# Kernel optimization log

Measured on AMD Instinct MI355X. Metric: run time of the kernel, lower is better.

Reference implementation:

```python
import jax, jax.numpy as jnp
import numpy as np

B, L, D = 2, 4096, 1024
H, DK, DV = 4, 256, 256
CONV_K = 4
FIR_KS = (1, 3, 7, 15)
GQP = 128
NS = len(FIR_KS) + 2  # fir scales + delta path + direct value path
GIN = GQP + NS
GH = max(8, GIN)
CHUNK = 32
FLOOR = 0.02  # step 0 -> floor_start


def l2norm(x):
    return x * jax.lax.rsqrt(jnp.sum(x * x, -1, keepdims=True) + 1e-6)


def dw_causal_conv(x, w):
    # x: (B, L, C), w: (C, K) depthwise causal conv (ShortConvolution / FIR)
    K = w.shape[1]
    y = jax.lax.conv_general_dilated(
        jnp.moveaxis(x, 1, 2), w[:, None, :], (1,), [(K - 1, 0)],
        feature_group_count=w.shape[0],
        dimension_numbers=("NCH", "OIH", "NCH"))
    return jnp.moveaxis(y, 1, 2)


def delta_rule_chunkwise(q, k, v, beta):
    # q,k: (b,h,L,dk)  v: (b,h,L,dv)  beta: (b,h,L);  L % CHUNK == 0
    b, h, Lp, dk = q.shape
    dv = v.shape[-1]
    n = Lp // CHUNK
    q = l2norm(q)
    k = l2norm(k)
    v = v * beta[..., None]
    kb = k * beta[..., None]
    rs = lambda t: t.reshape(b, h, n, CHUNK, -1)
    q, k, v, kb = rs(q), rs(k), rs(v), rs(kb)
    tri = jnp.triu(jnp.ones((CHUNK, CHUNK), bool), 0)       # incl diag
    tri_s = jnp.triu(jnp.ones((CHUNK, CHUNK), bool), 1)     # strict upper
    # inv = -(k_beta k^T) masked to strictly-lower
    inv = -jnp.where(tri, 0.0, jnp.einsum('bhncd,bhned->bhnce', kb, k))
    # forward substitution: (I - A)^{-1} - I for strictly lower A
    for i in range(1, CHUNK):
        row = inv[:, :, :, i, :]                              # (b,h,n,C)
        upd = jnp.einsum('bhnk,bhnkj->bhnj', row, inv)        # zero for j>=i
        inv = inv.at[:, :, :, i, :].add(upd)
    inv = inv + jnp.eye(CHUNK, dtype=inv.dtype)
    inv = inv.astype(jnp.bfloat16).astype(q.dtype)
    u = inv @ v                                               # (b,h,n,C,dv)
    w = inv @ kb                                              # (b,h,n,C,dk)
    mv = lambda t: jnp.moveaxis(t, 2, 0)                      # -> (n,b,h,C,d)
    S0 = jnp.zeros((b, h, dk, dv), q.dtype)

    def step(S, xs):
        q_i, k_i, u_i, w_i = xs
        attn = jnp.where(tri_s, 0.0, q_i @ jnp.swapaxes(k_i, -1, -2))
        u_t = u_i - w_i @ S
        o = q_i @ S + attn @ u_t
        S = S + jnp.swapaxes(k_i, -1, -2) @ u_t
        return S, o

    _, out = jax.lax.scan(step, S0, (mv(q), mv(k), mv(u), mv(w)))
    return jnp.moveaxis(out, 0, 2).reshape(b, h, Lp, dv)


def rmsnorm(x, w, eps=1e-5):
    return x * jax.lax.rsqrt(jnp.mean(x * x, -1, keepdims=True) + eps) * w


def _dirac_fir(key, channels, k):
    w = jnp.zeros((channels, k), jnp.float32).at[:, -1].set(1.0)
    return w + 0.01 * jax.random.normal(key, (channels, k), jnp.float32)


def setup_inputs():
    key = jax.random.key(0)
    ks = jax.random.split(key, 24)
    sc = 0.02
    C = H * DV
    b2 = jnp.zeros((NS,), jnp.float32).at[-1].set(1.0)  # identity-path bias
    return {
        "hidden_states": jax.random.normal(ks[0], (B, L, D), jnp.float32),
        "Wq": jax.random.normal(ks[1], (D, H * DK), jnp.float32) * sc,
        "Wk": jax.random.normal(ks[2], (D, H * DK), jnp.float32) * sc,
        "Wv": jax.random.normal(ks[3], (D, H * DV), jnp.float32) * sc,
        "Wb": jax.random.normal(ks[4], (D, H), jnp.float32) * sc,
        "conv_q_w": jax.random.normal(ks[5], (H * DK, CONV_K), jnp.float32) * 0.1,
        "conv_k_w": jax.random.normal(ks[6], (H * DK, CONV_K), jnp.float32) * 0.1,
        "conv_v_w": jax.random.normal(ks[7], (H * DV, CONV_K), jnp.float32) * 0.1,
        "fir_w0": _dirac_fir(ks[8], C, FIR_KS[0]),
        "fir_w1": _dirac_fir(ks[9], C, FIR_KS[1]),
        "fir_w2": _dirac_fir(ks[10], C, FIR_KS[2]),
        "fir_w3": _dirac_fir(ks[11], C, FIR_KS[3]),
        "Wqg": jax.random.normal(ks[12], (D, GQP), jnp.float32) * sc,
        "bqg": jnp.zeros((GQP,), jnp.float32),
        "Wf1": jax.random.normal(ks[13], (GIN, GH), jnp.float32) * sc,
        "bf1": jnp.zeros((GH,), jnp.float32),
        "Wf2": jax.random.normal(ks[14], (GH, NS), jnp.float32) * sc,
        "bf2": b2,
        "log_temp": jnp.zeros((H,), jnp.float32),
        "o_norm_w": jnp.ones((DV,), jnp.float32),
        "Wo": jax.random.normal(ks[15], (H * DV, D), jnp.float32) * sc,
    }


def reference(hidden_states, Wq, Wk, Wv, Wb, conv_q_w, conv_k_w, conv_v_w,
              fir_w0, fir_w1, fir_w2, fir_w3, Wqg, bqg, Wf1, bf1, Wf2, bf2,
              log_temp, o_norm_w, Wo):
    x = hidden_states
    # projections + causal ShortConvolution with SiLU (qk_activation='silu')
    q = jax.nn.silu(dw_causal_conv(x @ Wq, conv_q_w))
    k = jax.nn.silu(dw_causal_conv(x @ Wk, conv_k_w))
    v = jax.nn.silu(dw_causal_conv(x @ Wv, conv_v_w))
    q = q.reshape(B, L, H, DK)
    k = k.reshape(B, L, H, DK)
    v_direct = v.reshape(B, L, H, DV)
    beta = jax.nn.sigmoid(x @ Wb)  # (B,L,H)
    bh = lambda t: jnp.swapaxes(t, 1, 2)  # (B,L,H,d) -> (B,H,L,d)
    delta_bh = delta_rule_chunkwise(bh(q), bh(k), bh(v_direct), jnp.swapaxes(beta, 1, 2))
    delta_out = jnp.swapaxes(delta_bh, 1, 2)  # (B,L,H,DV)
    # multi-scale depthwise causal FIR branches on the value stream
    v_flat = v_direct.reshape(B, L, H * DV)
    firs = [dw_causal_conv(v_flat, w).reshape(B, L, H, DV)
            for w in (fir_w0, fir_w1, fir_w2, fir_w3)]
    streams = jnp.stack(firs + [delta_out, v_direct], axis=3)  # (B,L,H,NS,DV)
    # query-conditioned summary router
    summaries = jnp.mean(streams, axis=-1)                     # (B,L,H,NS)
    qg = x @ Wqg + bqg                                         # (B,L,GQP)
    qg = jnp.broadcast_to(qg[:, :, None, :], (B, L, H, GQP))
    gate_in = jnp.concatenate([qg, summaries], axis=-1)        # (B,L,H,GIN)
    hmid = jax.nn.gelu(gate_in @ Wf1 + bf1, approximate=False)
    logits = (hmid @ Wf2 + bf2) / jnp.exp(log_temp)[None, None, :, None]
    p = jax.nn.softmax(logits, axis=-1)
    p = p * (1.0 - NS * FLOOR) + FLOOR                          # prob floor
    fused = jnp.einsum('blhs,blhsd->blhd', p, streams)
    o = rmsnorm(fused, o_norm_w)
    return o.reshape(B, L, H * DV) @ Wo
```

## Files before the change

kernel.cpp:

```cpp
#include <hip/hip_runtime.h>
#include <hip/hip_bf16.h>
#include <math.h>

#define B_ 2
#define L_ 4096
#define D_ 1024
#define H_ 4
#define DK_ 256
#define BL_ 8192
#define C_ 1024
#define NCH_ 128
#define GQP_c 128
#define NS_c 6
#define GIN_c 134
#define GH_c 134

typedef __attribute__((ext_vector_type(8))) short short8;
typedef __attribute__((ext_vector_type(4))) float f32x4;

__device__ __forceinline__ float block_sum256(float v, float* red) {
  int t = threadIdx.x;
  #pragma unroll
  for (int o = 32; o > 0; o >>= 1) v += __shfl_down(v, o, 64);
  __syncthreads();
// ... 142 lines not shown
  const float* xr = x + (size_t)row * D_;
  float acc = 0.f;
  for (int k = lane; k < D_; k += 64) acc += xr[k] * Wb[(k << 2) + h];
  #pragma unroll
  for (int o = 32; o > 0; o >>= 1) acc += __shfl_down(acc, o, 64);
  if (lane == 0) beta[(row << 2) + h] = 1.f / (1.f + expf(-acc));
}

__global__ __launch_bounds__(256) void precompute(const float* __restrict__ q,
    const float* __restrict__ k, const float* __restrict__ v,
    const float* __restrict__ beta,
    float* __restrict__ qn, float* __restrict__ kn,
    float* __restrict__ vb, float* __restrict__ kb) {
  __shared__ float red[4];
  int bid = blockIdx.x;
  int t = threadIdx.x;
  int b = bid >> 14;
  int h = (bid >> 12) & 3;
  int l = bid & (L_ - 1);
  size_t in_off = (((size_t)(b * L_ + l)) << 10) + (h << 8) + t;
  float qv = q[in_off], kv = k[in_off], vv = v[in_off];
  float sq = block_sum256(qv * qv, red);
  float sk = block_sum256(kv * kv, red);
  float rq = rsqrtf(sq + 1e-6f);
  float rk = rsqrtf(sk + 1e-6f);
  float bt = beta[((b * L_ + l) << 2) + h];
  size_t oo = ((size_t)bid << 8) + t;
  float knv = kv * rk;
  qn[oo] = qv * rq;
  kn[oo] = knv;
  vb[oo] = vv * bt;
  kb[oo] = knv * bt;
}

__global__ __launch_bounds__(256) void inv_attn(const float* __restrict__ qn,
    const float* kn, const float* __restrict__ kb,
    float* __restrict__ invb, __hip_bfloat16* __restrict__ att_bf,
    __hip_bfloat16* knT_bf) {
  __shared__ float kn_s[32][257];
  __shared__ float inv_s[32][33];
  int ci = blockIdx.x;
  int t = threadIdx.x;
  size_t base = ((size_t)ci) << 13;
  for (int e = t; e < 8192; e += 256) kn_s[e >> 8][e & 255] = kn[base + e];
  __syncthreads();
  {
    unsigned short tmp[32];
    #pragma unroll
    for (int j = 0; j < 32; ++j) tmp[j] = bf16bits(kn_s[j][t]);
    unsigned short* kd = (unsigned short*)knT_bf + (((size_t)ci) << 14) +
                         (size_t)(t >> 4) * 512 + (size_t)(t & 15) * 8;
    #pragma unroll
    for (int g = 0; g < 4; ++g) *(uint4*)(kd + g * 128) = ((const uint4*)tmp)[g];
  }
  {
    int r = t >> 3, kt = t & 7;
    const float4* qrow = (const float4*)(qn + base + (size_t)r * 256 + (kt << 5));
    unsigned short tmp[32];
    #pragma unroll
    for (int i = 0; i < 8; ++i) {
      float4 f = qrow[i];
      tmp[i * 4 + 0] = bf16bits(f.x); tmp[i * 4 + 1] = bf16bits(f.y);
      tmp[i * 4 + 2] = bf16bits(f.z); tmp[i * 4 + 3] = bf16bits(f.w);
    }
    unsigned short* qd = (unsigned short*)knT_bf + (((size_t)ci) << 14) + 8192 +
                         (size_t)(((r >> 4) << 3) + kt) * 512 + (size_t)(r & 15) * 8;
    #pragma unroll
    for (int g = 0; g < 4; ++g) *(uint4*)(qd + g * 128) = ((const uint4*)tmp)[g];
  }
  #pragma unroll
  for (int p = 0; p < 4; ++p) {
    int e = t + (p << 8);
    int i = e >> 5, j = e & 31;
    const float* kbi = kb + base + (i << 8);
    const float* qni = qn + base + (i << 8);
    float am = 0.f, aa = 0.f;
    for (int kk = 0; kk < 256; ++kk) {
      float knv = kn_s[j][kk];
      am += kbi[kk] * knv;
      aa += qni[kk] * knv;
    }
    inv_s[i][j] = (j < i) ? -am : 0.f;
    ((unsigned short*)att_bf)[((size_t)ci << 10) + (size_t)(i >> 4) * 512 +
        (size_t)((i & 15) + ((j >> 3) << 4)) * 8 + (j & 7)] =
        bf16bits((j <= i) ? aa : 0.f);
  }
  __syncthreads();
  for (int i = 1; i < 32; ++i) {
    float upd = 0.f;
    if (t < i) {
      for (int kk = t + 1; kk < i; ++kk) upd += inv_s[i][kk] * inv_s[kk][t];
    }
    __syncthreads();
    if (t < i) inv_s[i][t] += upd;
    __syncthreads();
  }
  #pragma unroll
  for (int p = 0; p < 4; ++p) {
    int e = t + (p << 8);
    int i = e >> 5, j = e & 31;
    float val = inv_s[i][j] + (i == j ? 1.f : 0.f);
    val = __bfloat162float(__float2bfloat16(val));
    invb[((size_t)ci << 10) + e] = val;
  }
}

__global__ __launch_bounds__(256) void uw_kernel(const float* __restrict__ invb,
    float* __restrict__ vb_u, float* kb_w, __hip_bfloat16* w_bf) {
  __shared__ float inv_s[32][33];
  __shared__ float tile[32][260];
  int ci = blockIdx.x, t = threadIdx.x;
  size_t base = ((size_t)ci) << 13;
  for (int e = t; e < 1024; e += 256) inv_s[e >> 5][e & 31] = invb[((size_t)ci << 10) + e];
  for (int ph = 0; ph < 2; ++ph) {
    const float* src = (ph == 0) ? vb_u : kb_w;
    __syncthreads();
    for (int f = t; f < 2048; f += 256) {
      int e = f << 2;
      *(float4*)&tile[e >> 8][e & 255] = *(const float4*)(src + base + e);
    }
    __syncthreads();
    int c4 = (t & 63) << 2;
    int ig = t >> 6;
    float4 acc[8];
    #pragma unroll
    for (int ii = 0; ii < 8; ++ii) acc[ii] = make_float4(0.f, 0.f, 0.f, 0.f);
    for (int j = 0; j < 32; ++j) {
      float4 v4 = *(const float4*)&tile[j][c4];
      #pragma unroll
      for (int ii = 0; ii < 8; ++ii) {
        float iv = inv_s[(ig << 3) + ii][j];
        acc[ii].x += iv * v4.x; acc[ii].y += iv * v4.y;
        acc[ii].z += iv * v4.z; acc[ii].w += iv * v4.w;
      }
    }
    #pragma unroll
    for (int ii = 0; ii < 8; ++ii) {
      int i = (ig << 3) + ii;
      if (ph == 0) {
        *(float4*)(vb_u + base + (i << 8) + c4) = acc[ii];
      } else {
        ushort4 o;
        o.x = bf16bits(-acc[ii].x); o.y = bf16bits(-acc[ii].y);
        o.z = bf16bits(-acc[ii].z); o.w = bf16bits(-acc[ii].w);
        unsigned short* wd = (unsigned short*)w_bf + (((size_t)ci) << 14) +
            (size_t)(((i >> 4) << 3) + (c4 >> 5)) * 512 +
            (size_t)((i & 15) + (((c4 >> 3) & 3) << 4)) * 8 + (c4 & 7);
        *(ushort4*)wd = o;
      }
    }
  }
}

__global__ __launch_bounds__(64, 1) void scan_kernel(
    const __hip_bfloat16* __restrict__ w_bf,
    const __hip_bfloat16* __restrict__ kq_bf,
    const __hip_bfloat16* __restrict__ att_bf,
    const float* __restrict__ u, float* __restrict__ dout) {
  __shared__ __align__(16) unsigned short Sim[2][2][16 * 264];
  __shared__ __align__(16) float UtT[16 * 36];
  int lane = threadIdx.x;
  int mlane = lane & 15, quad = lane >> 4;
  int bh = blockIdx.x & 7;
  int cb = blockIdx.x >> 3;
  int cbase = cb << 4;

  const unsigned short* wbase = (const unsigned short*)w_bf;
  const unsigned short* kqbase = (const unsigned short*)kq_bf;
  const unsigned short* abase = (const unsigned short*)att_bf;

  short8 Wr[16], Qr[16], Kr[16], Ar[2];
  float ur[8], urn[8];

  auto load_WQ = [&](int nc) {
    size_t cb14 = ((size_t)(bh * NCH_ + nc)) << 14;
    const short8* wg = (const short8*)(wbase + cb14 + (size_t)lane * 8);
    const short8* qg = (const short8*)(kqbase + cb14 + 8192 + (size_t)lane * 8);
    #pragma unroll
    for (int s = 0; s < 16; ++s) { Wr[s] = wg[s * 64]; Qr[s] = qg[s * 64]; }
  };
  auto load_K = [&](int nc) {
    size_t cb14 = ((size_t)(bh * NCH_ + nc)) << 14;
    const short8* kg = (const short8*)(kqbase + cb14 + (size_t)lane * 8);
    #pragma unroll
    for (int s = 0; s < 16; ++s) Kr[s] = kg[s * 64];
  };
  auto load_A = [&](int nc) {
    const short8* ag = (const short8*)(abase + (((size_t)(bh * NCH_ + nc)) << 10) +
                                       (size_t)lane * 8);
    Ar[0] = ag[0]; Ar[1] = ag[64];
  };
  auto load_u8 = [&](int nc, float* dst) {
    size_t cbf = ((size_t)(bh * NCH_ + nc)) << 13;
    const float* up = u + cbf + (size_t)(quad * 4) * 256 + cbase + mlane;
    #pragma unroll
    for (int tt = 0; tt < 2; ++tt)
      #pragma unroll
      for (int r = 0; r < 4; ++r) dst[tt * 4 + r] = up[(tt * 16 + r) * 256];
  };

  for (int e = lane; e < 16 * 264; e += 64) { Sim[0][0][e] = 0; Sim[0][1][e] = 0; }
  f32x4 accS[16];
  #pragma unroll
  for (int i = 0; i < 16; ++i) accS[i] = (f32x4){0.f, 0.f, 0.f, 0.f};

  load_WQ(0);
  load_K(0);
  load_A(0);
  load_u8(0, ur);

  for (int nc = 0; nc < NCH_; ++nc) {
    int cur = nc & 1, alt = cur ^ 1;
    int nn = nc + 1 < NCH_ ? nc + 1 : NCH_ - 1;

    f32x4 uh0 = (f32x4){ur[0], ur[1], ur[2], ur[3]};
    f32x4 uh1 = (f32x4){ur[4], ur[5], ur[6], ur[7]};
    f32x4 ul0 = (f32x4){0.f, 0.f, 0.f, 0.f}, ul1 = (f32x4){0.f, 0.f, 0.f, 0.f};
    f32x4 oh0 = (f32x4){0.f, 0.f, 0.f, 0.f}, oh1 = (f32x4){0.f, 0.f, 0.f, 0.f};
    f32x4 ol0 = (f32x4){0.f, 0.f, 0.f, 0.f}, ol1 = (f32x4){0.f, 0.f, 0.f, 0.f};
    #pragma unroll
    for (int kt = 0; kt < 8; ++kt) {
      short8 bhi = *(const short8*)&Sim[cur][0][mlane * 264 + kt * 32 + quad * 8];
      short8 blo = *(const short8*)&Sim[cur][1][mlane * 264 + kt * 32 + quad * 8];
      uh0 = __builtin_amdgcn_mfma_f32_16x16x32_bf16(Wr[kt], bhi, uh0, 0, 0, 0);
      ul0 = __builtin_amdgcn_mfma_f32_16x16x32_bf16(Wr[kt], blo, ul0, 0, 0, 0);
      uh1 = __builtin_amdgcn_mfma_f32_16x16x32_bf16(Wr[8 + kt], bhi, uh1, 0, 0, 0);
      ul1 = __builtin_amdgcn_mfma_f32_16x16x32_bf16(Wr[8 + kt], blo, ul1, 0, 0, 0);
      oh0 = __builtin_amdgcn_mfma_f32_16x16x32_bf16(Qr[kt], bhi, oh0, 0, 0, 0);
      ol0 = __builtin_amdgcn_mfma_f32_16x16x32_bf16(Qr[kt], blo, ol0, 0, 0, 0);
      oh1 = __builtin_amdgcn_mfma_f32_16x16x32_bf16(Qr[8 + kt], bhi, oh1, 0, 0, 0);
      ol1 = __builtin_amdgcn_mfma_f32_16x16x32_bf16(Qr[8 + kt], blo, ol1, 0, 0, 0);
    }
    f32x4 ut0 = uh0 + ul0, ut1 = uh1 + ul1;
    *(f32x4*)&UtT[mlane * 36 + quad * 4] = ut0;
    *(f32x4*)&UtT[mlane * 36 + 16 + quad * 4] = ut1;
    load_WQ(nn);
    load_u8(nn, urn);
    short8 but;
    {
      const float* up = &UtT[mlane * 36 + quad * 8];
      #pragma unroll
      for (int j = 0; j < 8; ++j) but[j] = (short)bf16bits(up[j]);
    }
    f32x4 o0 = oh0 + ol0, o1 = oh1 + ol1;
    o0 = __builtin_amdgcn_mfma_f32_16x16x32_bf16(Ar[0], but, o0, 0, 0, 0);
    o1 = __builtin_amdgcn_mfma_f32_16x16x32_bf16(Ar[1], but, o1, 0, 0, 0);
    load_A(nn);
    size_t cbf = ((size_t)(bh * NCH_ + nc)) << 13;
    float* op = dout + cbf + (size_t)(quad * 4) * 256 + cbase + mlane;
    #pragma unroll
    for (int r = 0; r < 4; ++r) { op[r * 256] = o0[r]; op[(16 + r) * 256] = o1[r]; }
    #pragma unroll
    for (int t2 = 0; t2 < 16; ++t2) {
      accS[t2] = __builtin_amdgcn_mfma_f32_16x16x32_bf16(Kr[t2], but, accS[t2], 0, 0, 0);
      unsigned short nh[4], nl[4];
      #pragma unroll
      for (int r = 0; r < 4; ++r) {
        float sv = accS[t2][r];
        unsigned short hb = bf16bits(sv);
        nh[r] = hb;
        nl[r] = bf16bits(sv - bits2f(hb));
      }
      *(uint2*)&Sim[alt][0][mlane * 264 + t2 * 16 + quad * 4] = *(const uint2*)nh;
      *(uint2*)&Sim[alt][1][mlane * 264 + t2 * 16 + quad * 4] = *(const uint2*)nl;
    }
    load_K(nn);
    #pragma unroll
    for (int r = 0; r < 8; ++r) ur[r] = urn[r];
  }
}

__global__ __launch_bounds__(256, 1) void gate_kernel(
    const float* __restrict__ v, const float* __restrict__ delta,
    const float* __restrict__ qgH,
    const float* __restrict__ fw0, const float* __restrict__ fw1T,
    const float* __restrict__ fw2T, const float* __restrict__ fw3T,
    const float* __restrict__ Wf1, const float* __restrict__ Wf2,
    const float* __restrict__ bf1, const float* __restrict__ bf2,
    const float* __restrict__ ltm, const float* __restrict__ onw,
    __hip_bfloat16* __restrict__ obf) {
  __shared__ float W1t[6][136];
  __shared__ float W2f[804];
  __shared__ float bf1s[136];
  int t = threadIdx.x;
  int wave = t >> 6, lane = t & 63;
  for (int e = t; e < 804; e += 256) {
    int s = e / 134, u = e - s * 134;
    W1t[s][u] = Wf1[(128 + s) * GH_c + u];
    W2f[e] = Wf2[e];
  }
  if (t < GH_c) bf1s[t] = bf1[t];
  __syncthreads();

  int bid = blockIdx.x;
  int bl0 = (((bid & 7) << 7) | (bid >> 3)) << 3;
  int b = bl0 >> 12;
  int h = wave;
  int c = (h << 8) + (lane << 2);

  float4 fw3r[15], fw2r[7], fw1r[3], fw0r;
  #pragma unroll
  for (int j = 0; j < 15; ++j) fw3r[j] = *(const float4*)(fw3T + (j << 10) + c);
  #pragma unroll
  for (int j = 0; j < 7; ++j) fw2r[j] = *(const float4*)(fw2T + (j << 10) + c);
  #pragma unroll
  for (int j = 0; j < 3; ++j) fw1r[j] = *(const float4*)(fw1T + (j << 10) + c);
  fw0r = *(const float4*)(fw0 + c);
  float4 ow = *(const float4*)(onw + (lane << 2));
  float itemp = expf(ltm[h]);
  float b2r[6];
  #pragma unroll
  for (int s = 0; s < 6; ++s) b2r[s] = bf2[s];
  int u3 = 128 + (lane < 6 ? lane : 0);

  auto gelu = [](float a) -> float {
    return 0.5f * a * (1.f + erff(a * 0.70710678f));
  };

  for (int tk = 0; tk < 8; ++tk) {
    int bl = bl0 + tk;
    int l = bl & (L_ - 1);
    float4 st0, st1, st2, st3, st4, st5;
    st1 = make_float4(0, 0, 0, 0);
    st2 = make_float4(0, 0, 0, 0);
    st3 = make_float4(0, 0, 0, 0);
    #pragma unroll
    for (int j = 0; j < 15; ++j) {
      int ll = l - 14 + j;
      float4 vj = make_float4(0, 0, 0, 0);
      if (ll >= 0) vj = *(const float4*)(v + ((((size_t)(b * L_ + ll)) << 10) + c));
      st3 = fma4(fw3r[j], vj, st3);
      if (j >= 8) st2 = fma4(fw2r[j - 8], vj, st2);
      if (j >= 12) st1 = fma4(fw1r[j - 12], vj, st1);
      if (j == 14) {
        st0 = make_float4(fw0r.x * vj.x, fw0r.y * vj.y, fw0r.z * vj.z, fw0r.w * vj.w);
        st5 = vj;
      }
    }
    st4 = *(const float4*)(delta + ((((size_t)((b * H_ + h) * L_ + l)) << 8) + (lane << 2)));

    float s0 = st0.x + st0.y + st0.z + st0.w;
    float s1 = st1.x + st1.y + st1.z + st1.w;
    float s2 = st2.x + st2.y + st2.z + st2.w;
    float s3 = st3.x + st3.y + st3.z + st3.w;
    float s4 = st4.x + st4.y + st4.z + st4.w;
    float s5 = st5.x + st5.y + st5.z + st5.w;
    #pragma unroll
    for (int o = 32; o > 0; o >>= 1) {
      s0 += __shfl_down(s0, o, 64); s1 += __shfl_down(s1, o, 64);
      s2 += __shfl_down(s2, o, 64); s3 += __shfl_down(s3, o, 64);
      s4 += __shfl_down(s4, o, 64); s5 += __shfl_down(s5, o, 64);
    }
    float ss_[6];
    ss_[0] = __shfl(s0, 0, 64) * (1.f / 256.f);
    ss_[1] = __shfl(s1, 0, 64) * (1.f / 256.f);
    ss_[2] = __shfl(s2, 0, 64) * (1.f / 256.f);
    ss_[3] = __shfl(s3, 0, 64) * (1.f / 256.f);
    ss_[4] = __shfl(s4, 0, 64) * (1.f / 256.f);
    ss_[5] = __shfl(s5, 0, 64) * (1.f / 256.f);

    const float* qr = qgH + ((size_t)bl << 8);
    float a0 = qr[lane] + bf1s[lane];
    float a1 = qr[64 + lane] + bf1s[64 + lane];
    float a2 = qr[u3] + bf1s[u3];
    #pragma unroll
    for (int s = 0; s < 6; ++s) {
      a0 = fmaf(W1t[s][lane], ss_[s], a0);
      a1 = fmaf(W1t[s][64 + lane], ss_[s], a1);
      a2 = fmaf(W1t[s][u3], ss_[s], a2);
    }
    float h0 = gelu(a0);
    float h1 = gelu(a1);
    float h2 = (lane < 6) ? gelu(a2) : 0.f;

    const float* w2a = W2f + lane * 6;
    const float* w2b = W2f + (64 + lane) * 6;
    const float* w2c = W2f + u3 * 6;
    float t0 = h0 * w2a[0] + h1 * w2b[0] + h2 * w2c[0];
    float t1 = h0 * w2a[1] + h1 * w2b[1] + h2 * w2c[1];
    float t2 = h0 * w2a[2] + h1 * w2b[2] + h2 * w2c[2];
    float t3 = h0 * w2a[3] + h1 * w2b[3] + h2 * w2c[3];
    float t4 = h0 * w2a[4] + h1 * w2b[4] + h2 * w2c[4];
    float t5 = h0 * w2a[5] + h1 * w2b[5] + h2 * w2c[5];
    #pragma unroll
    for (int o = 32; o > 0; o >>= 1) {
      t0 += __shfl_down(t0, o, 64); t1 += __shfl_down(t1, o, 64);
      t2 += __shfl_down(t2, o, 64); t3 += __shfl_down(t3, o, 64);
      t4 += __shfl_down(t4, o, 64); t5 += __shfl_down(t5, o, 64);
    }
    float p0, p1, p2, p3, p4, p5;
    if (lane == 0) {
      float l0v = (t0 + b2r[0]) / itemp, l1v = (t1 + b2r[1]) / itemp;
      float l2v = (t2 + b2r[2]) / itemp, l3v = (t3 + b2r[3]) / itemp;
      float l4v = (t4 + b2r[4]) / itemp, l5v = (t5 + b2r[5]) / itemp;
      float m = fmaxf(fmaxf(fmaxf(l0v, l1v), fmaxf(l2v, l3v)), fmaxf(l4v, l5v));
      float e0 = expf(l0v - m), e1 = expf(l1v - m), e2 = expf(l2v - m);
      float e3 = expf(l3v - m), e4 = expf(l4v - m), e5 = expf(l5v - m);
      float inv = 1.f / (e0 + e1 + e2 + e3 + e4 + e5);
      p0 = e0 * inv * 0.88f + 0.02f; p1 = e1 * inv * 0.88f + 0.02f;
      p2 = e2 * inv * 0.88f + 0.02f; p3 = e3 * inv * 0.88f + 0.02f;
      p4 = e4 * inv * 0.88f + 0.02f; p5 = e5 * inv * 0.88f + 0.02f;
    }
    p0 = __shfl(p0, 0, 64); p1 = __shfl(p1, 0, 64); p2 = __shfl(p2, 0, 64);
    p3 = __shfl(p3, 0, 64); p4 = __shfl(p4, 0, 64); p5 = __shfl(p5, 0, 64);

    float4 fu;
    fu.x = p0 * st0.x + p1 * st1.x + p2 * st2.x + p3 * st3.x + p4 * st4.x + p5 * st5.x;
    fu.y = p0 * st0.y + p1 * st1.y + p2 * st2.y + p3 * st3.y + p4 * st4.y + p5 * st5.y;
    fu.z = p0 * st0.z + p1 * st1.z + p2 * st2.z + p3 * st3.z + p4 * st4.z + p5 * st5.z;
    fu.w = p0 * st0.w + p1 * st1.w + p2 * st2.w + p3 * st3.w + p4 * st4.w + p5 * st5.w;
    float ssq = fu.x * fu.x + fu.y * fu.y + fu.z * fu.z + fu.w * fu.w;
    #pragma unroll
    for (int o = 32; o > 0; o >>= 1) ssq += __shfl_xor(ssq, o, 64);
    float sc = rsqrtf(ssq * (1.f / 256.f) + 1e-5f);
    ushort4 ob;
    ob.x = bf16bits(fu.x * sc * ow.x);
    ob.y = bf16bits(fu.y * sc * ow.y);
    ob.z = bf16bits(fu.z * sc * ow.z);
    ob.w = bf16bits(fu.w * sc * ow.w);
    *(ushort4*)((unsigned short*)obf + (((size_t)bl) << 10) + c) = ob;
  }
}

extern "C" void kernel_launch(void* const* d_in, const int* in_sizes, int n_in,
                              void* d_out, int out_size, void* d_ws, size_t ws_size,
                              hipStream_t stream) {
  const float* x   = (const float*)d_in[0];
  const float* Wq  = (const float*)d_in[1];
  const float* Wk  = (const float*)d_in[2];
  const float* Wv  = (const float*)d_in[3];
  const float* Wb  = (const float*)d_in[4];
  const float* cqw = (const float*)d_in[5];
  const float* ckw = (const float*)d_in[6];
  const float* cvw = (const float*)d_in[7];
  const float* fw0 = (const float*)d_in[8];
  const float* fw1 = (const float*)d_in[9];
  const float* fw2 = (const float*)d_in[10];
  const float* fw3 = (const float*)d_in[11];
  const float* Wqg = (const float*)d_in[12];
  const float* bqg = (const float*)d_in[13];
  const float* Wf1 = (const float*)d_in[14];
  const float* bf1 = (const float*)d_in[15];
  const float* Wf2 = (const float*)d_in[16];
  const float* bf2 = (const float*)d_in[17];
  const float* ltm = (const float*)d_in[18];
  const float* onw = (const float*)d_in[19];
  const float* Wo  = (const float*)d_in[20];
  float* out = (float*)d_out;
  float* ws = (float*)d_ws;

  const size_t BIG = (size_t)BL_ * C_;
  float* qpre = ws;
  float* kpre = ws + BIG;
  float* vpre = ws + 2 * BIG;
  float* qs   = ws + 3 * BIG;
  float* ks   = ws + 4 * BIG;
  float* vs   = ws + 5 * BIG;
  float* kbw  = ws + 6 * BIG;
  float* invb = ws + 7 * BIG;
  float* attb = invb + (size_t)1024 * 1024;
  float* beta = attb + (size_t)1024 * 1024;
  float* qg   = beta + (size_t)BL_ * H_;

  __hip_bfloat16* x_bf  = (__hip_bfloat16*)qs;
  __hip_bfloat16* wqT   = (__hip_bfloat16*)kbw;
  __hip_bfloat16* wkT   = wqT + (size_t)1024 * 1024;
  __hip_bfloat16* wvT   = wkT + (size_t)1024 * 1024;
  __hip_bfloat16* wqgT  = wvT + (size_t)1024 * 1024;
  __hip_bfloat16* woT   = (__hip_bfloat16*)kbw;
  __hip_bfloat16* gate_bf = (__hip_bfloat16*)qpre;
  __hip_bfloat16* knT_bf = (__hip_bfloat16*)kpre;
  __hip_bfloat16* w_bf   = (__hip_bfloat16*)kbw;
  __hip_bfloat16* att_bf = (__hip_bfloat16*)attb;
  float* scr   = attb + (size_t)600000;
  float* fw1T  = scr;
  float* fw2T  = scr + 3072;
  float* fw3T  = scr + 10240;

  float* qgH = ks;
  __hip_bfloat16* qg_bf  = (__hip_bfloat16*)(ks + (size_t)3 * 1024 * 1024);
  __hip_bfloat16* wf1qT  = (__hip_bfloat16*)(ks + (size_t)4 * 1024 * 1024);

  dim3 blk(256);
  f32_to_bf16_k<<<dim3(BL_ * D_ / 1024), blk, 0, stream>>>(x, x_bf);
  transpose_bf16<<<dim3(32, 32), blk, 0, stream>>>(Wq, wqT, D_, C_);
  transpose_bf16<<<dim3(32, 32), blk, 0, stream>>>(Wk, wkT, D_, C_);
  transpose_bf16<<<dim3(32, 32), blk, 0, stream>>>(Wv, wvT, D_, C_);
  transpose_bf16<<<dim3(4, 32), blk, 0, stream>>>(Wqg, wqgT, D_, GQP_c);
  small_transpose<<<dim3(16), blk, 0, stream>>>(fw1, fw1T, 1024, 3, 1024);
  small_transpose<<<dim3(32), blk, 0, stream>>>(fw2, fw2T, 1024, 7, 1024);
  small_transpose<<<dim3(64), blk, 0, stream>>>(fw3, fw3T, 1024, 15, 1024);
  gemm_bf16<<<dim3(8, 64), blk, 0, stream>>>(x_bf, wqT, nullptr, qpre, BL_, C_, D_);
  gemm_bf16<<<dim3(8, 64), blk, 0, stream>>>(x_bf, wkT, nullptr, kpre, BL_, C_, D_);
  gemm_bf16<<<dim3(8, 64), blk, 0, stream>>>(x_bf, wvT, nullptr, vpre, BL_, C_, D_);
  gemm_bf16<<<dim3(1, 64), blk, 0, stream>>>(x_bf, wqgT, bqg, qg, BL_, GQP_c, D_);
  beta_kernel<<<dim3(BL_), blk, 0, stream>>>(x, Wb, beta);
  conv_silu<<<dim3(BL_ * C_ / 256), blk, 0, stream>>>(qpre, cqw, qs);
  conv_silu<<<dim3(BL_ * C_ / 256), blk, 0, stream>>>(kpre, ckw, ks);
  conv_silu<<<dim3(BL_ * C_ / 256), blk, 0, stream>>>(vpre, cvw, vs);
  precompute<<<dim3(B_ * H_ * L_), blk, 0, stream>>>(qs, ks, vs, beta, qpre, kpre,
                                                     vpre, kbw);
  f32_to_bf16_k<<<dim3(BL_ * GQP_c / 1024), blk, 0, stream>>>(qg, qg_bf);
  wf1q_prep<<<dim3(128), blk, 0, stream>>>(Wf1, wf1qT);
  gemm_bf16<<<dim3(2, 64), blk, 0, stream>>>(qg_bf, wf1qT, nullptr, qgH, BL_, 256, 128);
  inv_attn<<<dim3(1024), blk, 0, stream>>>(qpre, kpre, kbw, invb, att_bf, knT_bf);
  uw_kernel<<<dim3(1024), blk, 0, stream>>>(invb, vpre, kbw, w_bf);
  scan_kernel<<<dim3(128), dim3(64), 0, stream>>>(w_bf, knT_bf, att_bf, vpre, qs);
  transpose_bf16<<<dim3(32, 32), blk, 0, stream>>>(Wo, woT, C_, D_);
  gate_kernel<<<dim3(1024), blk, 0, stream>>>(vs, qs, qgH, fw0, fw1T, fw2T, fw3T,
                                              Wf1, Wf2, bf1, bf2, ltm, onw, gate_bf);
  gemm_bf16<<<dim3(8, 64), blk, 0, stream>>>(gate_bf, woT, nullptr, out, BL_, D_, C_);
}
```

Measured before the change: 976.5 us.

## Process chunk pairs in scan using precomputed cross-chunk correction matrices

```diff
diff --git a/kernel.cpp b/kernel.cpp
--- a/kernel.cpp
+++ b/kernel.cpp
@@ -318,12 +318,53 @@
   }
 }
 
+__global__ __launch_bounds__(256) void mn_prep(
+    const __hip_bfloat16* __restrict__ w_bf, const __hip_bfloat16* __restrict__ kq_bf,
+    unsigned short* __restrict__ mn) {
+  __shared__ float wb_[32][260];
+  __shared__ float qb_[32][260];
+  __shared__ float ka_[256][33];
+  int p = blockIdx.x;
+  int bh = p >> 6, i = p & 63;
+  int ca = bh * NCH_ + 2 * i, cbk = ca + 1;
+  int t = threadIdx.x;
+  const unsigned short* wsrc = (const unsigned short*)w_bf + ((size_t)cbk << 14);
+  const unsigned short* qsrc = (const unsigned short*)kq_bf + ((size_t)cbk << 14) + 8192;
+  const unsigned short* ksrc = (const unsigned short*)kq_bf + ((size_t)ca << 14);
+  for (int e = t; e < 8192; e += 256) {
+    int s = e >> 9, ln = (e >> 3) & 63, j = e & 7;
+    int row = ((s >> 3) << 4) | (ln & 15);
+    int col = ((s & 7) << 5) | (((ln >> 4) & 3) << 3) | j;
+    wb_[row][col] = bits2f(wsrc[e]);
+    qb_[row][col] = bits2f(qsrc[e]);
+    int krow = (s << 4) | (ln & 15);
+    int kcol = (((ln >> 4) & 3) << 3) | j;
+    ka_[krow][kcol] = bits2f(ksrc[e]);
+  }
+  __syncthreads();
+  unsigned short* dst = mn + ((size_t)p << 11);
+  #pragma unroll
+  for (int g = 0; g < 8; ++g) {
+    int idx = g * 256 + t;
+    int which = idx >> 10;
+    int rc = idx & 1023;
+    int r = rc >> 5, ccol = rc & 31;
+    const float* src = which ? &qb_[r][0] : &wb_[r][0];
+    float acc = 0.f;
+    for (int d = 0; d < 256; ++d) acc = fmaf(src[d], ka_[d][ccol], acc);
+    int addr = ((r >> 4) << 9) + (((r & 15) | (((ccol >> 3) & 3) << 4)) << 3) + (ccol & 7);
+    dst[(which << 10) + addr] = bf16bits(acc);
+  }
+}
+
 __global__ __launch_bounds__(64, 1) void scan_kernel(
     const __hip_bfloat16* __restrict__ w_bf,
     const __hip_bfloat16* __restrict__ kq_bf,
     const __hip_bfloat16* __restrict__ att_bf,
+    const unsigned short* __restrict__ mn,
     const float* __restrict__ u, float* __restrict__ dout) {
-  __shared__ __align__(16) unsigned short Sim[2][2][16 * 264];
+  __shared__ __align__(16) unsigned short Shi[16 * 264];
+  __shared__ __align__(16) unsigned short Slo[16 * 264];
   __shared__ __align__(16) float UtT[16 * 36];
   int lane = threadIdx.x;
   int mlane = lane & 15, quad = lane >> 4;
@@ -335,59 +376,79 @@
   const unsigned short* kqbase = (const unsigned short*)kq_bf;
   const unsigned short* abase = (const unsigned short*)att_bf;
 
-  short8 Wr[16], Qr[16], Kr[16], Ar[2];
-  float ur[8], urn[8];
-
-  auto load_WQ = [&](int nc) {
-    size_t cb14 = ((size_t)(bh * NCH_ + nc)) << 14;
-    const short8* wg = (const short8*)(wbase + cb14 + (size_t)lane * 8);
-    const short8* qg = (const short8*)(kqbase + cb14 + 8192 + (size_t)lane * 8);
-    #pragma unroll
-    for (int s = 0; s < 16; ++s) { Wr[s] = wg[s * 64]; Qr[s] = qg[s * 64]; }
+  short8 Wr[16], Qr[16], Wb2[16], Qb2[16], Ka[16], Kb[16];
+  short8 Mr[2], Nr[2], Aa[2], Ab[2];
+  float ua[8], ub[8];
+
+  auto load_WQ = [&](int ci, short8* W, short8* Q) {
+    size_t c14 = ((size_t)ci) << 14;
+    const short8* wg = (const short8*)(wbase + c14 + (size_t)lane * 8);
+    const short8* qg = (const short8*)(kqbase + c14 + 8192 + (size_t)lane * 8);
+    #pragma unroll
+    for (int s = 0; s < 16; ++s) { W[s] = wg[s * 64]; Q[s] = qg[s * 64]; }
   };
-  auto load_K = [&](int nc) {
-    size_t cb14 = ((size_t)(bh * NCH_ + nc)) << 14;
-    const short8* kg = (const short8*)(kqbase + cb14 + (size_t)lane * 8);
-    #pragma unroll
-    for (int s = 0; s < 16; ++s) Kr[s] = kg[s * 64];
+  auto load_K = [&](int ci, short8* K) {
+    const short8* kg = (const short8*)(kqbase + (((size_t)ci) << 14) + (size_t)lane * 8);
+    #pragma unroll
+    for (int s = 0; s < 16; ++s) K[s] = kg[s * 64];
   };
-  auto load_A = [&](int nc) {
-    const short8* ag = (const short8*)(abase + (((size_t)(bh * NCH_ + nc)) << 10) +
+  auto load_MNA = [&](int pi) {
+    int ca = bh * NCH_ + 2 * pi, cbk = ca + 1;
+    const short8* mg = (const short8*)(mn + (((size_t)(bh * 64 + pi)) << 11) +
                                        (size_t)lane * 8);
-    Ar[0] = ag[0]; Ar[1] = ag[64];
+    Mr[0] = mg[0]; Mr[1] = mg[64];
+    Nr[0] = mg[128]; Nr[1] = mg[192];
+    const short8* aga = (const short8*)(abase + (((size_t)ca) << 10) + (size_t)lane * 8);
+    const short8* agb = (const short8*)(abase + (((size_t)cbk) << 10) + (size_t)lane * 8);
+    Aa[0] = aga[0]; Aa[1] = aga[64];
+    Ab[0] = agb[0]; Ab[1] = agb[64];
   };
-  auto load_u8 = [&](int nc, float* dst) {
-    size_t cbf = ((size_t)(bh * NCH_ + nc)) << 13;
+  auto load_u8 = [&](int ci, float* dst) {
+    size_t cbf = ((size_t)ci) << 13;
     const float* up = u + cbf + (size_t)(quad * 4) * 256 + cbase + mlane;
     #pragma unroll
     for (int tt = 0; tt < 2; ++tt)
       #pragma unroll
       for (int r = 0; r < 4; ++r) dst[tt * 4 + r] = up[(tt * 16 + r) * 256];
   };
-
-  for (int e = lane; e < 16 * 264; e += 64) { Sim[0][0][e] = 0; Sim[0][1][e] = 0; }
+  auto relayout_ut = [&](f32x4 u0, f32x4 u1) -> short8 {
+    *(f32x4*)&UtT[mlane * 36 + quad * 4] = u0;
+    *(f32x4*)&UtT[mlane * 36 + 16 + quad * 4] = u1;
+    short8 bt;
+    const float* up = &UtT[mlane * 36 + quad * 8];
+    #pragma unroll
+    for (int j = 0; j < 8; ++j) bt[j] = (short)bf16bits(up[j]);
+    return bt;
+  };
+  auto store_o = [&](int ci, f32x4 o0, f32x4 o1) {
+    size_t cbf = ((size_t)ci) << 13;
+    float* op = dout + cbf + (size_t)(quad * 4) * 256 + cbase + mlane;
+    #pragma unroll
+    for (int r = 0; r < 4; ++r) { op[r * 256] = o0[r]; op[(16 + r) * 256] = o1[r]; }
+  };
+
+  for (int e = lane; e < 16 * 264; e += 64) { Shi[e] = 0; Slo[e] = 0; }
   f32x4 accS[16];
   #pragma unroll
   for (int i = 0; i < 16; ++i) accS[i] = (f32x4){0.f, 0.f, 0.f, 0.f};
 
-  load_WQ(0);
-  load_K(0);
-  load_A(0);
-  load_u8(0, ur);
-
-  for (int nc = 0; nc < NCH_; ++nc) {
-    int cur = nc & 1, alt = cur ^ 1;
-    int nn = nc + 1 < NCH_ ? nc + 1 : NCH_ - 1;
-
-    f32x4 uh0 = (f32x4){ur[0], ur[1], ur[2], ur[3]};
-    f32x4 uh1 = (f32x4){ur[4], ur[5], ur[6], ur[7]};
+  load_WQ(bh * NCH_, Wr, Qr);
+  load_u8(bh * NCH_, ua);
+  load_MNA(0);
+
+  for (int pi = 0; pi < 64; ++pi) {
+    int ca = bh * NCH_ + 2 * pi, cbk = ca + 1;
+    int pn = pi + 1 < 64 ? pi + 1 : 63;
+
+    f32x4 uh0 = (f32x4){ua[0], ua[1], ua[2], ua[3]};
+    f32x4 uh1 = (f32x4){ua[4], ua[5], ua[6], ua[7]};
     f32x4 ul0 = (f32x4){0.f, 0.f, 0.f, 0.f}, ul1 = (f32x4){0.f, 0.f, 0.f, 0.f};
     f32x4 oh0 = (f32x4){0.f, 0.f, 0.f, 0.f}, oh1 = (f32x4){0.f, 0.f, 0.f, 0.f};
     f32x4 ol0 = (f32x4){0.f, 0.f, 0.f, 0.f}, ol1 = (f32x4){0.f, 0.f, 0.f, 0.f};
     #pragma unroll
     for (int kt = 0; kt < 8; ++kt) {
-      short8 bhi = *(const short8*)&Sim[cur][0][mlane * 264 + kt * 32 + quad * 8];
-      short8 blo = *(const short8*)&Sim[cur][1][mlane * 264 + kt * 32 + quad * 8];
+      short8 bhi = *(const short8*)&Shi[mlane * 264 + kt * 32 + quad * 8];
+      short8 blo = *(const short8*)&Slo[mlane * 264 + kt * 32 + quad * 8];
       uh0 = __builtin_amdgcn_mfma_f32_16x16x32_bf16(Wr[kt], bhi, uh0, 0, 0, 0);
       ul0 = __builtin_amdgcn_mfma_f32_16x16x32_bf16(Wr[kt], blo, ul0, 0, 0, 0);
       uh1 = __builtin_amdgcn_mfma_f32_16x16x32_bf16(Wr[8 + kt], bhi, uh1, 0, 0, 0);
@@ -397,28 +458,50 @@
       oh1 = __builtin_amdgcn_mfma_f32_16x16x32_bf16(Qr[8 + kt], bhi, oh1, 0, 0, 0);
       ol1 = __builtin_amdgcn_mfma_f32_16x16x32_bf16(Qr[8 + kt], blo, ol1, 0, 0, 0);
     }
-    f32x4 ut0 = uh0 + ul0, ut1 = uh1 + ul1;
-    *(f32x4*)&UtT[mlane * 36 + quad * 4] = ut0;
-    *(f32x4*)&UtT[mlane * 36 + 16 + quad * 4] = ut1;
-    load_WQ(nn);
-    load_u8(nn, urn);
-    short8 but;
-    {
-      const float* up = &UtT[mlane * 36 + quad * 8];
-      #pragma unroll
-      for (int j = 0; j < 8; ++j) but[j] = (short)bf16bits(up[j]);
-    }
-    f32x4 o0 = oh0 + ol0, o1 = oh1 + ol1;
-    o0 = __builtin_amdgcn_mfma_f32_16x16x32_bf16(Ar[0], but, o0, 0, 0, 0);
-    o1 = __builtin_amdgcn_mfma_f32_16x16x32_bf16(Ar[1], but, o1, 0, 0, 0);
-    load_A(nn);
-    size_t cbf = ((size_t)(bh * NCH_ + nc)) << 13;
-    float* op = dout + cbf + (size_t)(quad * 4) * 256 + cbase + mlane;
-    #pragma unroll
-    for (int r = 0; r < 4; ++r) { op[r * 256] = o0[r]; op[(16 + r) * 256] = o1[r]; }
+    load_WQ(cbk, Wb2, Qb2);
+    load_u8(cbk, ub);
+    load_K(ca, Ka);
+    short8 buta = relayout_ut(uh0 + ul0, uh1 + ul1);
+    f32x4 oa0 = oh0 + ol0, oa1 = oh1 + ol1;
+    oa0 = __builtin_amdgcn_mfma_f32_16x16x32_bf16(Aa[0], buta, oa0, 0, 0, 0);
+    oa1 = __builtin_amdgcn_mfma_f32_16x16x32_bf16(Aa[1], buta, oa1, 0, 0, 0);
+    store_o(ca, oa0, oa1);
+
+    f32x4 vh0 = (f32x4){ub[0], ub[1], ub[2], ub[3]};
+    f32x4 vh1 = (f32x4){ub[4], ub[5], ub[6], ub[7]};
+    f32x4 vl0 = (f32x4){0.f, 0.f, 0.f, 0.f}, vl1 = (f32x4){0.f, 0.f, 0.f, 0.f};
+    f32x4 ph0 = (f32x4){0.f, 0.f, 0.f, 0.f}, ph1 = (f32x4){0.f, 0.f, 0.f, 0.f};
+    f32x4 pl0 = (f32x4){0.f, 0.f, 0.f, 0.f}, pl1 = (f32x4){0.f, 0.f, 0.f, 0.f};
+    #pragma unroll
+    for (int kt = 0; kt < 8; ++kt) {
+      short8 bhi = *(const short8*)&Shi[mlane * 264 + kt * 32 + quad * 8];
+      short8 blo = *(const short8*)&Slo[mlane * 264 + kt * 32 + quad * 8];
+      vh0 = __builtin_amdgcn_mfma_f32_16x16x32_bf16(Wb2[kt], bhi, vh0, 0, 0, 0);
+      vl0 = __builtin_amdgcn_mfma_f32_16x16x32_bf16(Wb2[kt], blo, vl0, 0, 0, 0);
+      vh1 = __builtin_amdgcn_mfma_f32_16x16x32_bf16(Wb2[8 + kt], bhi, vh1, 0, 0, 0);
+      vl1 = __builtin_amdgcn_mfma_f32_16x16x32_bf16(Wb2[8 + kt], blo, vl1, 0, 0, 0);
+      ph0 = __builtin_amdgcn_mfma_f32_16x16x32_bf16(Qb2[kt], bhi, ph0, 0, 0, 0);
+      pl0 = __builtin_amdgcn_mfma_f32_16x16x32_bf16(Qb2[kt], blo, pl0, 0, 0, 0);
+      ph1 = __builtin_amdgcn_mfma_f32_16x16x32_bf16(Qb2[8 + kt], bhi, ph1, 0, 0, 0);
+      pl1 = __builtin_amdgcn_mfma_f32_16x16x32_bf16(Qb2[8 + kt], blo, pl1, 0, 0, 0);
+    }
+    load_K(cbk, Kb);
+    load_WQ(bh * NCH_ + 2 * pn, Wr, Qr);
+    load_u8(bh * NCH_ + 2 * pn, ua);
+    vh0 = __builtin_amdgcn_mfma_f32_16x16x32_bf16(Mr[0], buta, vh0, 0, 0, 0);
+    vh1 = __builtin_amdgcn_mfma_f32_16x16x32_bf16(Mr[1], buta, vh1, 0, 0, 0);
+    ph0 = __builtin_amdgcn_mfma_f32_16x16x32_bf16(Nr[0], buta, ph0, 0, 0, 0);
+    ph1 = __builtin_amdgcn_mfma_f32_16x16x32_bf16(Nr[1], buta, ph1, 0, 0, 0);
+    short8 butb = relayout_ut(vh0 + vl0, vh1 + vl1);
+    f32x4 ob0 = ph0 + pl0, ob1 = ph1 + pl1;
+    ob0 = __builtin_amdgcn_mfma_f32_16x16x32_bf16(Ab[0], butb, ob0, 0, 0, 0);
+    ob1 = __builtin_amdgcn_mfma_f32_16x16x32_bf16(Ab[1], butb, ob1, 0, 0, 0);
+    store_o(cbk, ob0, ob1);
+    load_MNA(pn);
     #pragma unroll
     for (int t2 = 0; t2 < 16; ++t2) {
-      accS[t2] = __builtin_amdgcn_mfma_f32_16x16x32_bf16(Kr[t2], but, accS[t2], 0, 0, 0);
+      accS[t2] = __builtin_amdgcn_mfma_f32_16x16x32_bf16(Ka[t2], buta, accS[t2], 0, 0, 0);
+      accS[t2] = __builtin_amdgcn_mfma_f32_16x16x32_bf16(Kb[t2], butb, accS[t2], 0, 0, 0);
       unsigned short nh[4], nl[4];
       #pragma unroll
       for (int r = 0; r < 4; ++r) {
@@ -427,12 +510,9 @@
         nh[r] = hb;
         nl[r] = bf16bits(sv - bits2f(hb));
       }
-      *(uint2*)&Sim[alt][0][mlane * 264 + t2 * 16 + quad * 4] = *(const uint2*)nh;
-      *(uint2*)&Sim[alt][1][mlane * 264 + t2 * 16 + quad * 4] = *(const uint2*)nl;
-    }
-    load_K(nn);
-    #pragma unroll
-    for (int r = 0; r < 8; ++r) ur[r] = urn[r];
+      *(uint2*)&Shi[mlane * 264 + t2 * 16 + quad * 4] = *(const uint2*)nh;
+      *(uint2*)&Slo[mlane * 264 + t2 * 16 + quad * 4] = *(const uint2*)nl;
+    }
   }
 }
 
@@ -638,6 +718,7 @@
   __hip_bfloat16* knT_bf = (__hip_bfloat16*)kpre;
   __hip_bfloat16* w_bf   = (__hip_bfloat16*)kbw;
   __hip_bfloat16* att_bf = (__hip_bfloat16*)attb;
+  unsigned short* mnbuf = (unsigned short*)invb;
   float* scr   = attb + (size_t)600000;
   float* fw1T  = scr;
   float* fw2T  = scr + 3072;
@@ -671,7 +752,9 @@
   gemm_bf16<<<dim3(2, 64), blk, 0, stream>>>(qg_bf, wf1qT, nullptr, qgH, BL_, 256, 128);
   inv_attn<<<dim3(1024), blk, 0, stream>>>(qpre, kpre, kbw, invb, att_bf, knT_bf);
   uw_kernel<<<dim3(1024), blk, 0, stream>>>(invb, vpre, kbw, w_bf);
-  scan_kernel<<<dim3(128), dim3(64), 0, stream>>>(w_bf, knT_bf, att_bf, vpre, qs);
+  mn_prep<<<dim3(512), blk, 0, stream>>>(w_bf, knT_bf, mnbuf);
+  scan_kernel<<<dim3(128), dim3(64), 0, stream>>>(w_bf, knT_bf, att_bf, mnbuf,
+                                                  vpre, qs);
   transpose_bf16<<<dim3(32, 32), blk, 0, stream>>>(Wo, woT, C_, D_);
   gate_kernel<<<dim3(1024), blk, 0, stream>>>(vs, qs, qgH, fw0, fw1T, fw2T, fw3T,
                                               Wf1, Wf2, bf1, bf2, ltm, onw, gate_bf);
```

After: 1.224 ms. +25.3%, slower.

## Warp-specialize scan kernel with producer wave staging chunks into LDS

Applied to the files above, without the earlier changes.

```diff
diff --git a/kernel.cpp b/kernel.cpp
--- a/kernel.cpp
+++ b/kernel.cpp
@@ -318,14 +318,17 @@
   }
 }
 
-__global__ __launch_bounds__(64, 1) void scan_kernel(
+__global__ __launch_bounds__(128, 1) void scan_kernel(
     const __hip_bfloat16* __restrict__ w_bf,
     const __hip_bfloat16* __restrict__ kq_bf,
     const __hip_bfloat16* __restrict__ att_bf,
     const float* __restrict__ u, float* __restrict__ dout) {
-  __shared__ __align__(16) unsigned short Sim[2][2][16 * 264];
+  __shared__ __align__(16) unsigned short stg[2][25600];
+  __shared__ __align__(16) unsigned short Shi[16 * 264];
+  __shared__ __align__(16) unsigned short Slo[16 * 264];
   __shared__ __align__(16) float UtT[16 * 36];
-  int lane = threadIdx.x;
+  int tid = threadIdx.x;
+  int wave = tid >> 6, lane = tid & 63;
   int mlane = lane & 15, quad = lane >> 4;
   int bh = blockIdx.x & 7;
   int cb = blockIdx.x >> 3;
@@ -335,27 +338,23 @@
   const unsigned short* kqbase = (const unsigned short*)kq_bf;
   const unsigned short* abase = (const unsigned short*)att_bf;
 
-  short8 Wr[16], Qr[16], Kr[16], Ar[2];
+  auto stage_chunk = [&](int nc, int buf) {
+    size_t ci = (size_t)(bh * NCH_ + nc);
+    const unsigned short* wg = wbase + (ci << 14) + lane * 8;
+    const unsigned short* kg = kqbase + (ci << 14) + lane * 8;
+    const unsigned short* qg = kqbase + (ci << 14) + 8192 + lane * 8;
+    const unsigned short* ag = abase + (ci << 10) + lane * 8;
+    unsigned short* l = &stg[buf][lane * 8];
+    #pragma unroll
+    for (int s = 0; s < 16; ++s) {
+      gload_lds16(wg + s * 512, l + s * 512);
+      gload_lds16(kg + s * 512, l + 8192 + s * 512);
+      gload_lds16(qg + s * 512, l + 16384 + s * 512);
+    }
+    gload_lds16(ag, l + 24576);
+    gload_lds16(ag + 512, l + 25088);
+  };
   float ur[8], urn[8];
-
-  auto load_WQ = [&](int nc) {
-    size_t cb14 = ((size_t)(bh * NCH_ + nc)) << 14;
-    const short8* wg = (const short8*)(wbase + cb14 + (size_t)lane * 8);
-    const short8* qg = (const short8*)(kqbase + cb14 + 8192 + (size_t)lane * 8);
-    #pragma unroll
-    for (int s = 0; s < 16; ++s) { Wr[s] = wg[s * 64]; Qr[s] = qg[s * 64]; }
-  };
-  auto load_K = [&](int nc) {
-    size_t cb14 = ((size_t)(bh * NCH_ + nc)) << 14;
-    const short8* kg = (const short8*)(kqbase + cb14 + (size_t)lane * 8);
-    #pragma unroll
-    for (int s = 0; s < 16; ++s) Kr[s] = kg[s * 64];
-  };
-  auto load_A = [&](int nc) {
-    const short8* ag = (const short8*)(abase + (((size_t)(bh * NCH_ + nc)) << 10) +
-                                       (size_t)lane * 8);
-    Ar[0] = ag[0]; Ar[1] = ag[64];
-  };
   auto load_u8 = [&](int nc, float* dst) {
     size_t cbf = ((size_t)(bh * NCH_ + nc)) << 13;
     const float* up = u + cbf + (size_t)(quad * 4) * 256 + cbase + mlane;
@@ -365,74 +364,90 @@
       for (int r = 0; r < 4; ++r) dst[tt * 4 + r] = up[(tt * 16 + r) * 256];
   };
 
-  for (int e = lane; e < 16 * 264; e += 64) { Sim[0][0][e] = 0; Sim[0][1][e] = 0; }
   f32x4 accS[16];
-  #pragma unroll
-  for (int i = 0; i < 16; ++i) accS[i] = (f32x4){0.f, 0.f, 0.f, 0.f};
-
-  load_WQ(0);
-  load_K(0);
-  load_A(0);
-  load_u8(0, ur);
+  if (wave == 1) {
+    stage_chunk(0, 0);
+    asm volatile("s_waitcnt vmcnt(0)" ::: "memory");
+  } else {
+    for (int e = lane; e < 16 * 264; e += 64) { Shi[e] = 0; Slo[e] = 0; }
+    #pragma unroll
+    for (int i = 0; i < 16; ++i) accS[i] = (f32x4){0.f, 0.f, 0.f, 0.f};
+    load_u8(0, ur);
+  }
+  __syncthreads();
 
   for (int nc = 0; nc < NCH_; ++nc) {
-    int cur = nc & 1, alt = cur ^ 1;
-    int nn = nc + 1 < NCH_ ? nc + 1 : NCH_ - 1;
-
-    f32x4 uh0 = (f32x4){ur[0], ur[1], ur[2], ur[3]};
-    f32x4 uh1 = (f32x4){ur[4], ur[5], ur[6], ur[7]};
-    f32x4 ul0 = (f32x4){0.f, 0.f, 0.f, 0.f}, ul1 = (f32x4){0.f, 0.f, 0.f, 0.f};
-    f32x4 oh0 = (f32x4){0.f, 0.f, 0.f, 0.f}, oh1 = (f32x4){0.f, 0.f, 0.f, 0.f};
-    f32x4 ol0 = (f32x4){0.f, 0.f, 0.f, 0.f}, ol1 = (f32x4){0.f, 0.f, 0.f, 0.f};
-    #pragma unroll
-    for (int kt = 0; kt < 8; ++kt) {
-      short8 bhi = *(const short8*)&Sim[cur][0][mlane * 264 + kt * 32 + quad * 8];
-      short8 blo = *(const short8*)&Sim[cur][1][mlane * 264 + kt * 32 + quad * 8];
-      uh0 = __builtin_amdgcn_mfma_f32_16x16x32_bf16(Wr[kt], bhi, uh0, 0, 0, 0);
-      ul0 = __builtin_amdgcn_mfma_f32_16x16x32_bf16(Wr[kt], blo, ul0, 0, 0, 0);
-      uh1 = __builtin_amdgcn_mfma_f32_16x16x32_bf16(Wr[8 + kt], bhi, uh1, 0, 0, 0);
-      ul1 = __builtin_amdgcn_mfma_f32_16x16x32_bf16(Wr[8 + kt], blo, ul1, 0, 0, 0);
-      oh0 = __builtin_amdgcn_mfma_f32_16x16x32_bf16(Qr[kt], bhi, oh0, 0, 0, 0);
-      ol0 = __builtin_amdgcn_mfma_f32_16x16x32_bf16(Qr[kt], blo, ol0, 0, 0, 0);
-      oh1 = __builtin_amdgcn_mfma_f32_16x16x32_bf16(Qr[8 + kt], bhi, oh1, 0, 0, 0);
-      ol1 = __builtin_amdgcn_mfma_f32_16x16x32_bf16(Qr[8 + kt], blo, ol1, 0, 0, 0);
-    }
-    f32x4 ut0 = uh0 + ul0, ut1 = uh1 + ul1;
-    *(f32x4*)&UtT[mlane * 36 + quad * 4] = ut0;
-    *(f32x4*)&UtT[mlane * 36 + 16 + quad * 4] = ut1;
-    load_WQ(nn);
-    load_u8(nn, urn);
-    short8 but;
-    {
-      const float* up = &UtT[mlane * 36 + quad * 8];
-      #pragma unroll
-      for (int j = 0; j < 8; ++j) but[j] = (short)bf16bits(up[j]);
-    }
-    f32x4 o0 = oh0 + ol0, o1 = oh1 + ol1;
-    o0 = __builtin_amdgcn_mfma_f32_16x16x32_bf16(Ar[0], but, o0, 0, 0, 0);
-    o1 = __builtin_amdgcn_mfma_f32_16x16x32_bf16(Ar[1], but, o1, 0, 0, 0);
-    load_A(nn);
-    size_t cbf = ((size_t)(bh * NCH_ + nc)) << 13;
-    float* op = dout + cbf + (size_t)(quad * 4) * 256 + cbase + mlane;
-    #pragma unroll
-    for (int r = 0; r < 4; ++r) { op[r * 256] = o0[r]; op[(16 + r) * 256] = o1[r]; }
-    #pragma unroll
-    for (int t2 = 0; t2 < 16; ++t2) {
-      accS[t2] = __builtin_amdgcn_mfma_f32_16x16x32_bf16(Kr[t2], but, accS[t2], 0, 0, 0);
-      unsigned short nh[4], nl[4];
-      #pragma unroll
-      for (int r = 0; r < 4; ++r) {
-        float sv = accS[t2][r];
-        unsigned short hb = bf16bits(sv);
-        nh[r] = hb;
-        nl[r] = bf16bits(sv - bits2f(hb));
+    int cur = nc & 1;
+    if (wave == 1) {
+      if (nc + 1 < NCH_) stage_chunk(nc + 1, cur ^ 1);
+      asm volatile("s_waitcnt vmcnt(0)" ::: "memory");
+    } else {
+      int nn = nc + 1 < NCH_ ? nc + 1 : NCH_ - 1;
+      const unsigned short* SW = &stg[cur][0];
+      const unsigned short* SK = &stg[cur][8192];
+      const unsigned short* SQ = &stg[cur][16384];
+      const unsigned short* SA = &stg[cur][24576];
+
+      f32x4 uh0 = (f32x4){ur[0], ur[1], ur[2], ur[3]};
+      f32x4 uh1 = (f32x4){ur[4], ur[5], ur[6], ur[7]};
+      f32x4 ul0 = (f32x4){0.f, 0.f, 0.f, 0.f}, ul1 = (f32x4){0.f, 0.f, 0.f, 0.f};
+      f32x4 oh0 = (f32x4){0.f, 0.f, 0.f, 0.f}, oh1 = (f32x4){0.f, 0.f, 0.f, 0.f};
+      f32x4 ol0 = (f32x4){0.f, 0.f, 0.f, 0.f}, ol1 = (f32x4){0.f, 0.f, 0.f, 0.f};
+      #pragma unroll
+      for (int kt = 0; kt < 8; ++kt) {
+        short8 bhi = *(const short8*)&Shi[mlane * 264 + kt * 32 + quad * 8];
+        short8 blo = *(const short8*)&Slo[mlane * 264 + kt * 32 + quad * 8];
+        short8 w0 = *(const short8*)&SW[kt * 512 + lane * 8];
+        short8 w1 = *(const short8*)&SW[(8 + kt) * 512 + lane * 8];
+        short8 q0 = *(const short8*)&SQ[kt * 512 + lane * 8];
+        short8 q1 = *(const short8*)&SQ[(8 + kt) * 512 + lane * 8];
+        uh0 = __builtin_amdgcn_mfma_f32_16x16x32_bf16(w0, bhi, uh0, 0, 0, 0);
+        ul0 = __builtin_amdgcn_mfma_f32_16x16x32_bf16(w0, blo, ul0, 0, 0, 0);
+        uh1 = __builtin_amdgcn_mfma_f32_16x16x32_bf16(w1, bhi, uh1, 0, 0, 0);
+        ul1 = __builtin_amdgcn_mfma_f32_16x16x32_bf16(w1, blo, ul1, 0, 0, 0);
+        oh0 = __builtin_amdgcn_mfma_f32_16x16x32_bf16(q0, bhi, oh0, 0, 0, 0);
+        ol0 = __builtin_amdgcn_mfma_f32_16x16x32_bf16(q0, blo, ol0, 0, 0, 0);
+        oh1 = __builtin_amdgcn_mfma_f32_16x16x32_bf16(q1, bhi, oh1, 0, 0, 0);
+        ol1 = __builtin_amdgcn_mfma_f32_16x16x32_bf16(q1, blo, ol1, 0, 0, 0);
       }
-      *(uint2*)&Sim[alt][0][mlane * 264 + t2 * 16 + quad * 4] = *(const uint2*)nh;
-      *(uint2*)&Sim[alt][1][mlane * 264 + t2 * 16 + quad * 4] = *(const uint2*)nl;
-    }
-    load_K(nn);
-    #pragma unroll
-    for (int r = 0; r < 8; ++r) ur[r] = urn[r];
+      f32x4 ut0 = uh0 + ul0, ut1 = uh1 + ul1;
+      *(f32x4*)&UtT[mlane * 36 + quad * 4] = ut0;
+      *(f32x4*)&UtT[mlane * 36 + 16 + quad * 4] = ut1;
+      load_u8(nn, urn);
+      short8 but;
+      {
+        const float* up = &UtT[mlane * 36 + quad * 8];
+        #pragma unroll
+        for (int j = 0; j < 8; ++j) but[j] = (short)bf16bits(up[j]);
+      }
+      short8 a0 = *(const short8*)&SA[lane * 8];
+      short8 a1 = *(const short8*)&SA[512 + lane * 8];
+      f32x4 o0 = oh0 + ol0, o1 = oh1 + ol1;
+      o0 = __builtin_amdgcn_mfma_f32_16x16x32_bf16(a0, but, o0, 0, 0, 0);
+      o1 = __builtin_amdgcn_mfma_f32_16x16x32_bf16(a1, but, o1, 0, 0, 0);
+      size_t cbf = ((size_t)(bh * NCH_ + nc)) << 13;
+      float* op = dout + cbf + (size_t)(quad * 4) * 256 + cbase + mlane;
+      #pragma unroll
+      for (int r = 0; r < 4; ++r) { op[r * 256] = o0[r]; op[(16 + r) * 256] = o1[r]; }
+      #pragma unroll
+      for (int t2 = 0; t2 < 16; ++t2) {
+        short8 kA = *(const short8*)&SK[t2 * 512 + lane * 8];
+        accS[t2] = __builtin_amdgcn_mfma_f32_16x16x32_bf16(kA, but, accS[t2], 0, 0, 0);
+        unsigned short nh[4], nl[4];
+        #pragma unroll
+        for (int r = 0; r < 4; ++r) {
+          float sv = accS[t2][r];
+          unsigned short hb = bf16bits(sv);
+          nh[r] = hb;
+          nl[r] = bf16bits(sv - bits2f(hb));
+        }
+        *(uint2*)&Shi[mlane * 264 + t2 * 16 + quad * 4] = *(const uint2*)nh;
+        *(uint2*)&Slo[mlane * 264 + t2 * 16 + quad * 4] = *(const uint2*)nl;
+      }
+      #pragma unroll
+      for (int r = 0; r < 8; ++r) ur[r] = urn[r];
+    }
+    __syncthreads();
   }
 }
 
@@ -671,7 +686,7 @@
   gemm_bf16<<<dim3(2, 64), blk, 0, stream>>>(qg_bf, wf1qT, nullptr, qgH, BL_, 256, 128);
   inv_attn<<<dim3(1024), blk, 0, stream>>>(qpre, kpre, kbw, invb, att_bf, knT_bf);
   uw_kernel<<<dim3(1024), blk, 0, stream>>>(invb, vpre, kbw, w_bf);
-  scan_kernel<<<dim3(128), dim3(64), 0, stream>>>(w_bf, knT_bf, att_bf, vpre, qs);
+  scan_kernel<<<dim3(128), dim3(128), 0, stream>>>(w_bf, knT_bf, att_bf, vpre, qs);
   transpose_bf16<<<dim3(32, 32), blk, 0, stream>>>(Wo, woT, C_, D_);
   gate_kernel<<<dim3(1024), blk, 0, stream>>>(vs, qs, qgH, fw0, fw1T, fw2T, fw3T,
                                               Wf1, Wf2, bf1, bf2, ltm, onw, gate_bf);
```

Measured after the change: 1.016 ms. 1.04x slower.
